# Kernel optimization log

Measured on AMD Instinct MI355X. Metric: run time of the kernel, lower is better.

The kernel has to match this reference:

```python
import jax, jax.numpy as jnp
import numpy as np

EPS = 1e-6
K_STEPS = 4
USE_GATING = True


def layer_norm(x, gamma, beta):
    mu = jnp.mean(x, axis=-1, keepdims=True)
    var = jnp.mean(jnp.square(x - mu), axis=-1, keepdims=True)
    return (x - mu) * jax.lax.rsqrt(var + EPS) * gamma + beta


def setup_inputs() -> dict:
    key = jax.random.key(0)
    B, L, D, H = 4, 4096, 2048, 8192
    ks = jax.random.split(key, 16)
    s = 0.02
    return {
        "x": jax.random.normal(ks[0], (B, L, D), dtype=jnp.float32),
        "in_gamma": jnp.ones((D,), jnp.float32),
        "in_beta": jnp.zeros((D,), jnp.float32),
        "agg_w": jax.random.normal(ks[1], (D, D), jnp.float32) * s,
        "agg_b": jnp.zeros((D,), jnp.float32),
        "pn_gamma": jnp.ones((D,), jnp.float32),
        "pn_beta": jnp.zeros((D,), jnp.float32),
        "d1_w": jax.random.normal(ks[2], (D, H), jnp.float32) * s,
        "d1_b": jnp.zeros((H,), jnp.float32),
        "d2_w": jax.random.normal(ks[3], (H, D), jnp.float32) * s,
        "d2_b": jnp.zeros((D,), jnp.float32),
        "bc_w": jax.random.normal(ks[4], (D, D), jnp.float32) * s,
        "bc_b": jnp.zeros((D,), jnp.float32),
        "gate_w": jax.random.normal(ks[5], (D, D), jnp.float32) * s,
        "gate_b": jnp.zeros((D,), jnp.float32),
        "out_gamma": jnp.ones((D,), jnp.float32),
        "out_beta": jnp.zeros((D,), jnp.float32),
    }


def reference(x, in_gamma, in_beta, agg_w, agg_b, pn_gamma, pn_beta,
              d1_w, d1_b, d2_w, d2_b, bc_w, bc_b, gate_w, gate_b,
              out_gamma, out_beta):
    # Input norm over the full sequence, then extract last-position summary.
    x_norm = layer_norm(x, in_gamma, in_beta)              # [B, L, D]
    thought = x_norm[:, -1, :] @ agg_w + agg_b             # [B, D]

    # Iterative pre-norm MLP thought refinement (fixed small k -> unrolled).
    for _ in range(K_STEPS):
        t = layer_norm(thought, pn_gamma, pn_beta)
        t = jax.nn.gelu(t @ d1_w + d1_b, approximate=False)
        thought = thought + (t @ d2_w + d2_b)

    # Broadcast refined thought back to every position.
    broadcast = (thought @ bc_w + bc_b)[:, None, :]        # [B, 1, D]

    if USE_GATING:
        gate = jax.nn.sigmoid(x @ gate_w + gate_b)         # [B, L, D]
        out = x + gate * broadcast
    else:
        out = x + broadcast
    return layer_norm(out, out_gamma, out_beta)
```

## Files before the change

kernel.cpp:

```cpp
#include <hip/hip_runtime.h>
#include <stdint.h>

typedef __attribute__((ext_vector_type(8))) short short8;
typedef __attribute__((ext_vector_type(4))) float f32x4;
typedef __attribute__((ext_vector_type(4))) unsigned short us4;

__device__ inline unsigned short f2bf(float f) {
    unsigned u = __float_as_uint(f);
    u = (u + 0x7FFFu + ((u >> 16) & 1u)) >> 16;
    return (unsigned short)u;
}

__device__ inline float bf2f(unsigned short u) {
    return __uint_as_float(((unsigned)u) << 16);
}

__device__ inline float gelu_f(float v) {
    return 0.5f * v * (1.0f + erff(v * 0.70710678118654752f));
}

__device__ inline void gload_lds16(const unsigned short* g, const unsigned short* l) {
    __builtin_amdgcn_global_load_lds(
        (const __attribute__((address_space(1))) unsigned int*)(g),
        (__attribute__((address_space(3))) unsigned int*)(l),
        16, 0, 0);
}

__global__ __launch_bounds__(256) void cvt_x_kernel(const float* __restrict__ in,
                                                    unsigned short* __restrict__ out, int n4) {
    int i = blockIdx.x * 256 + threadIdx.x;
    if (i >= n4) return;
    float4 v = reinterpret_cast<const float4*>(in)[i];
    us4 o = { f2bf(v.x), f2bf(v.y), f2bf(v.z), f2bf(v.w) };
    reinterpret_cast<us4*>(out)[i] = o;
}

__global__ __launch_bounds__(256) void transpose_w_kernel(const float* __restrict__ W,
                                                          unsigned short* __restrict__ WT,
                                                          int K, int N) {
    __shared__ float tile[32][33];
    int bn = blockIdx.x * 32;
    int bk = blockIdx.y * 32;
    int tx = threadIdx.x & 31;
    int ty = threadIdx.x >> 5;
#pragma unroll
    for (int j = 0; j < 32; j += 8)
        tile[ty + j][tx] = W[(long long)(bk + ty + j) * N + bn + tx];
    __syncthreads();
#pragma unroll
    for (int j = 0; j < 32; j += 8)
        WT[(long long)(bn + ty + j) * K + bk + tx] = f2bf(tile[tx][ty + j]);
}

__device__ inline void block_reduce2(float& s, float& q) {
#pragma unroll
    for (int o = 32; o > 0; o >>= 1) {
        s += __shfl_xor(s, o, 64);
        q += __shfl_xor(q, o, 64);
    }
    __shared__ float sh[8];
    __syncthreads();
    int w = threadIdx.x >> 6;
    if ((threadIdx.x & 63) == 0) { sh[w] = s; sh[4 + w] = q; }
    __syncthreads();
    s = (sh[0] + sh[1]) + (sh[2] + sh[3]);
    q = (sh[4] + sh[5]) + (sh[6] + sh[7]);
}

__global__ __launch_bounds__(256) void ln_rows_kernel(const float* __restrict__ in, long long in_stride,
                                                      float* __restrict__ out, long long out_stride,
                                                      const float* __restrict__ gamma,
                                                      const float* __restrict__ beta) {
    const float* p = in + (long long)blockIdx.x * in_stride;
    float* q = out + (long long)blockIdx.x * out_stride;
    int t = threadIdx.x;
    float4 a = reinterpret_cast<const float4*>(p)[t];
    float4 c = reinterpret_cast<const float4*>(p)[t + 256];
    float s  = (a.x + a.y) + (a.z + a.w) + (c.x + c.y) + (c.z + c.w);
    float ss = a.x*a.x + a.y*a.y + a.z*a.z + a.w*a.w
             + c.x*c.x + c.y*c.y + c.z*c.z + c.w*c.w;
    block_reduce2(s, ss);
    const float inv = 1.0f / 2048.0f;
    float mu = s * inv;
    float var = ss * inv - mu * mu;
    float rs = rsqrtf(var + 1e-6f);
    float4 g0 = reinterpret_cast<const float4*>(gamma)[t];
    float4 g1 = reinterpret_cast<const float4*>(gamma)[t + 256];
    float4 b0 = reinterpret_cast<const float4*>(beta)[t];
    float4 b1 = reinterpret_cast<const float4*>(beta)[t + 256];
    float4 o0, o1;
    o0.x = (a.x - mu) * rs * g0.x + b0.x;
    o0.y = (a.y - mu) * rs * g0.y + b0.y;
    o0.z = (a.z - mu) * rs * g0.z + b0.z;
    o0.w = (a.w - mu) * rs * g0.w + b0.w;
    o1.x = (c.x - mu) * rs * g1.x + b1.x;
    o1.y = (c.y - mu) * rs * g1.y + b1.y;
    o1.z = (c.z - mu) * rs * g1.z + b1.z;
    o1.w = (c.w - mu) * rs * g1.w + b1.w;
    reinterpret_cast<float4*>(q)[t] = o0;
    reinterpret_cast<float4*>(q)[t + 256] = o1;
}

template<int MODE>
__global__ __launch_bounds__(256) void gemv4f_kernel(const float* __restrict__ src, long long sstride,
                                                     const float* __restrict__ gamma,
                                                     const float* __restrict__ beta,
                                                     const float* __restrict__ W,
                                                     const float* __restrict__ bias,
                                                     float* __restrict__ out,
                                                     int K, int N, int KC) {
    __shared__ float sA[4][128];
    const int tid = threadIdx.x;
    const int k0 = blockIdx.y * KC;

    float mu[4], rsd[4];
    if (MODE == 1) {
#pragma unroll
        for (int r = 0; r < 4; ++r) {
            const float* p = src + r * sstride;
            float s = 0.f, q = 0.f;
            for (int k = tid; k < K; k += 256) { float v = p[k]; s += v; q += v * v; }
            block_reduce2(s, q);
            float m = s / K;
            mu[r] = m;
            rsd[r] = rsqrtf(q / K - m * m + 1e-6f);
        }
    }
    for (int idx = tid; idx < 4 * KC; idx += 256) {
        int r = idx / KC, k = idx - r * KC;
        float v = src[r * sstride + k0 + k];
        if (MODE == 1) v = (v - mu[r]) * rsd[r] * gamma[k0 + k] + beta[k0 + k];
        if (MODE == 2) v = gelu_f(v);
        sA[r][k] = v;
    }
    __syncthreads();

    const int n4 = blockIdx.x * 256 + tid;
    const int n = n4 * 4;
    const float4* W4 = reinterpret_cast<const float4*>(W);
    float4 a0 = {0.f, 0.f, 0.f, 0.f}, a1 = a0, a2 = a0, a3 = a0;
#pragma unroll 4
    for (int k = 0; k < KC; ++k) {
        float4 w = W4[((long long)(k0 + k) * N + n) >> 2];
        float c0 = sA[0][k], c1 = sA[1][k], c2 = sA[2][k], c3 = sA[3][k];
        a0.x = fmaf(c0, w.x, a0.x); a0.y = fmaf(c0, w.y, a0.y);
        a0.z = fmaf(c0, w.z, a0.z); a0.w = fmaf(c0, w.w, a0.w);
        a1.x = fmaf(c1, w.x, a1.x); a1.y = fmaf(c1, w.y, a1.y);
        a1.z = fmaf(c1, w.z, a1.z); a1.w = fmaf(c1, w.w, a1.w);
        a2.x = fmaf(c2, w.x, a2.x); a2.y = fmaf(c2, w.y, a2.y);
        a2.z = fmaf(c2, w.z, a2.z); a2.w = fmaf(c2, w.w, a2.w);
        a3.x = fmaf(c3, w.x, a3.x); a3.y = fmaf(c3, w.y, a3.y);
        a3.z = fmaf(c3, w.z, a3.z); a3.w = fmaf(c3, w.w, a3.w);
    }
    if (blockIdx.y == 0) {
        float4 b = reinterpret_cast<const float4*>(bias)[n4];
        a0.x += b.x; a0.y += b.y; a0.z += b.z; a0.w += b.w;
        a1.x += b.x; a1.y += b.y; a1.z += b.z; a1.w += b.w;
        a2.x += b.x; a2.y += b.y; a2.z += b.z; a2.w += b.w;
        a3.x += b.x; a3.y += b.y; a3.z += b.z; a3.w += b.w;
    }
    atomicAdd(&out[n + 0], a0.x); atomicAdd(&out[n + 1], a0.y);
    atomicAdd(&out[n + 2], a0.z); atomicAdd(&out[n + 3], a0.w);
    atomicAdd(&out[N + n + 0], a1.x); atomicAdd(&out[N + n + 1], a1.y);
    atomicAdd(&out[N + n + 2], a1.z); atomicAdd(&out[N + n + 3], a1.w);
    atomicAdd(&out[2 * N + n + 0], a2.x); atomicAdd(&out[2 * N + n + 1], a2.y);
    atomicAdd(&out[2 * N + n + 2], a2.z); atomicAdd(&out[2 * N + n + 3], a2.w);
    atomicAdd(&out[3 * N + n + 0], a3.x); atomicAdd(&out[3 * N + n + 1], a3.y);
    atomicAdd(&out[3 * N + n + 2], a3.z); atomicAdd(&out[3 * N + n + 3], a3.w);
}

#define BK 64
__global__ __launch_bounds__(512, 4) void gate_gemm_kernel(const unsigned short* __restrict__ A,
                                                           const unsigned short* __restrict__ BT,
                                                           const float* __restrict__ gate_b,
                                                           const float* __restrict__ bcast,
                                                           float* __restrict__ pre,
                                                           int M, int N, int K) {
    extern __shared__ unsigned short lds[];
    const int tid = threadIdx.x;
    const int lane = tid & 63;
    const int wave = tid >> 6;
    const int wm = wave >> 2;
    const int wn = wave & 3;
    const int bn0 = blockIdx.x * 128;
    const int bm0 = blockIdx.y * 128;
    const int NT = K / BK;

    const int ch0 = tid, ch1 = tid + 512;
    const int r0 = ch0 >> 3, c0s = (ch0 & 7) ^ (r0 & 7);
    const int r1 = ch1 >> 3, c1s = (ch1 & 7) ^ (r1 & 7);
    const int srcoff0 = r0 * K + c0s * 8;
    const int srcoff1 = r1 * K + c1s * 8;
    const int ldso0 = ch0 * 8;
    const int ldso1 = ch1 * 8;

    const unsigned short* Abase = A + (long long)bm0 * K;
    const unsigned short* Bbase = BT + (long long)bn0 * K;

#define STAGE_A(buf, t)  do { \
        const unsigned short* g = Abase + (t) * BK; \
        const unsigned short* d = &lds[(buf) * 8192]; \
        gload_lds16(g + srcoff0, d + ldso0); \
        gload_lds16(g + srcoff1, d + ldso1); } while (0)
#define STAGE_B(buf, t)  do { \
        const unsigned short* g = Bbase + (t) * BK; \
        const unsigned short* d = &lds[16384 + (buf) * 8192]; \
        gload_lds16(g + srcoff0, d + ldso0); \
        gload_lds16(g + srcoff1, d + ldso1); } while (0)

    f32x4 acc[4][2];
#pragma unroll
    for (int i = 0; i < 4; ++i)
#pragma unroll
        for (int j = 0; j < 2; ++j)
#pragma unroll
            for (int r = 0; r < 4; ++r) acc[i][j][r] = 0.f;

    const int r16 = lane & 15, kq = lane >> 4;

    STAGE_A(0, 0); STAGE_B(0, 0);
    asm volatile("s_waitcnt vmcnt(0)" ::: "memory");
    __builtin_amdgcn_s_barrier();

    for (int t = 0; t < NT; ++t) {
        const int p = t & 1;
        const int u = t + 1;
        const int a_base = p * 8192;
        const int b_base = 16384 + p * 8192;

        if (u < NT) { STAGE_A(1 - p, u); STAGE_B(1 - p, u); }
        __builtin_amdgcn_sched_barrier(0);

        short8 bf[2][2];
#pragma unroll
        for (int ni = 0; ni < 2; ++ni) {
            const int rl = wn * 32 + ni * 16 + r16;
#pragma unroll
            for (int kk = 0; kk < 2; ++kk)
                bf[ni][kk] = *reinterpret_cast<const short8*>(
                    &lds[b_base + rl * 64 + (((kk << 2) | kq) ^ (rl & 7)) * 8]);
        }
        short8 af[4][2];
#pragma unroll
        for (int mi = 0; mi < 4; ++mi) {
            const int rl = wm * 64 + mi * 16 + r16;
#pragma unroll
            for (int kk = 0; kk < 2; ++kk)
                af[mi][kk] = *reinterpret_cast<const short8*>(
                    &lds[a_base + rl * 64 + (((kk << 2) | kq) ^ (rl & 7)) * 8]);
        }
        __builtin_amdgcn_s_setprio(1);
#pragma unroll
        for (int mi = 0; mi < 4; ++mi)
#pragma unroll
            for (int ni = 0; ni < 2; ++ni)
#pragma unroll
                for (int kk = 0; kk < 2; ++kk)
                    acc[mi][ni] = __builtin_amdgcn_mfma_f32_16x16x32_bf16(
                        af[mi][kk], bf[ni][kk], acc[mi][ni], 0, 0, 0);
        __builtin_amdgcn_s_setprio(0);
        asm volatile("s_waitcnt vmcnt(0)" ::: "memory");
        __builtin_amdgcn_s_barrier();
    }

    const int bnum = bm0 >> 12;
    const float* bc_row = bcast + (long long)bnum * N;
#pragma unroll
    for (int mi = 0; mi < 4; ++mi) {
        const int row = bm0 + wm * 64 + mi * 16 + kq * 4;
#pragma unroll
        for (int ni = 0; ni < 2; ++ni) {
            const int col = bn0 + wn * 32 + ni * 16 + r16;
            const float gb = gate_b[col];
            const float bc = bc_row[col];
#pragma unroll
            for (int r = 0; r < 4; ++r) {
                const long long off = (long long)(row + r) * N + col;
                const float v = acc[mi][ni][r] + gb;
                const float g = 1.0f / (1.0f + __expf(-v));
                pre[off] = bf2f(A[off]) + g * bc;
            }
        }
    }
}
#undef STAGE_A
#undef STAGE_B

extern "C" void kernel_launch(void* const* d_in, const int* in_sizes, int n_in,
                              void* d_out, int out_size, void* d_ws, size_t ws_size,
                              hipStream_t stream) {
    const float* x         = (const float*)d_in[0];
    const float* in_gamma  = (const float*)d_in[1];
    const float* in_beta   = (const float*)d_in[2];
    const float* agg_w     = (const float*)d_in[3];
    const float* agg_b     = (const float*)d_in[4];
    const float* pn_gamma  = (const float*)d_in[5];
    const float* pn_beta   = (const float*)d_in[6];
    const float* d1_w      = (const float*)d_in[7];
    const float* d1_b      = (const float*)d_in[8];
    const float* d2_w      = (const float*)d_in[9];
    const float* d2_b      = (const float*)d_in[10];
    const float* bc_w      = (const float*)d_in[11];
    const float* bc_b      = (const float*)d_in[12];
    const float* gate_w    = (const float*)d_in[13];
    const float* gate_b    = (const float*)d_in[14];
    const float* out_gamma = (const float*)d_in[15];
    const float* out_beta  = (const float*)d_in[16];

    const int B = 4, L = 4096, D = 2048, H = 8192;
    const int M = B * L;
    float* out = (float*)d_out;

    char* ws = (char*)d_ws;
    unsigned short* xb  = (unsigned short*)ws;
    unsigned short* gwT = (unsigned short*)(ws + 67108864);
    float* tbuf  = (float*)(ws + 75497472);
    float* bcast = tbuf + 4 * D;
    float* hbuf0 = bcast + 4 * D;

    static bool attr_done = false;
    if (!attr_done) {
        hipFuncSetAttribute((const void*)gate_gemm_kernel,
                            hipFuncAttributeMaxDynamicSharedMemorySize, 65536);
        attr_done = true;
    }

    hipMemsetAsync(tbuf, 0, (4 * D + 4 * D + 4 * 4 * H) * sizeof(float), stream);

    gemv4f_kernel<1><<<dim3(D / 1024, 64), dim3(256), 0, stream>>>(
        x + (long long)(L - 1) * D, (long long)L * D, in_gamma, in_beta,
        agg_w, agg_b, tbuf, D, D, 32);

    for (int s = 0; s < 4; ++s) {
        float* hbuf = hbuf0 + s * 4 * H;
        gemv4f_kernel<1><<<dim3(H / 1024, 32), dim3(256), 0, stream>>>(
            tbuf, (long long)D, pn_gamma, pn_beta, d1_w, d1_b, hbuf, D, H, 64);
        gemv4f_kernel<2><<<dim3(D / 1024, 128), dim3(256), 0, stream>>>(
            hbuf, (long long)H, nullptr, nullptr, d2_w, d2_b, tbuf, H, D, 64);
    }
    gemv4f_kernel<0><<<dim3(D / 1024, 64), dim3(256), 0, stream>>>(
        tbuf, (long long)D, nullptr, nullptr, bc_w, bc_b, bcast, D, D, 32);

    cvt_x_kernel<<<dim3((M * D / 4) / 256), dim3(256), 0, stream>>>(x, xb, M * D / 4);
    transpose_w_kernel<<<dim3(D / 32, D / 32), dim3(256), 0, stream>>>(gate_w, gwT, D, D);

    gate_gemm_kernel<<<dim3(D / 128, M / 128), dim3(512), 65536, stream>>>(
        xb, gwT, gate_b, bcast, out, M, D, D);

    ln_rows_kernel<<<dim3(M), dim3(256), 0, stream>>>(
        out, (long long)D, out, (long long)D, out_gamma, out_beta);
}
```

Measured before the change: 539.0 us.

## Replace d1 atomics with partial-sum buffers and remap gate GEMM blocks per XCD

The d1 GEMV now writes per-K-chunk partial sums with plain stores instead of atomicAdd. The following d2 GEMV reduces those 32 partials, adds the bias and applies GELU while loading. This also shrinks the memset, since the hidden buffers no longer need zeroing. Separately, the gate GEMM uses a 1D grid with a block-index swizzle so consecutive blocks on the same XCD share A rows, aiming for better L2 reuse; the cost is more reads in the d2 prologue.

```diff
diff --git a/kernel.cpp b/kernel.cpp
--- a/kernel.cpp
+++ b/kernel.cpp
@@ -101,10 +101,11 @@
     reinterpret_cast<float4*>(q)[t + 256] = o1;
 }
 
-template<int MODE>
+template<int MODE, int PARTIAL>
 __global__ __launch_bounds__(256) void gemv4f_kernel(const float* __restrict__ src, long long sstride,
                                                      const float* __restrict__ gamma,
                                                      const float* __restrict__ beta,
+                                                     const float* __restrict__ srcbias, int nY,
                                                      const float* __restrict__ W,
                                                      const float* __restrict__ bias,
                                                      float* __restrict__ out,
@@ -113,8 +114,8 @@
     const int tid = threadIdx.x;
     const int k0 = blockIdx.y * KC;
 
-    float mu[4], rsd[4];
     if (MODE == 1) {
+        float mu[4], rsd[4];
 #pragma unroll
         for (int r = 0; r < 4; ++r) {
             const float* p = src + r * sstride;
@@ -125,13 +126,25 @@
             mu[r] = m;
             rsd[r] = rsqrtf(q / K - m * m + 1e-6f);
         }
-    }
-    for (int idx = tid; idx < 4 * KC; idx += 256) {
-        int r = idx / KC, k = idx - r * KC;
-        float v = src[r * sstride + k0 + k];
-        if (MODE == 1) v = (v - mu[r]) * rsd[r] * gamma[k0 + k] + beta[k0 + k];
-        if (MODE == 2) v = gelu_f(v);
-        sA[r][k] = v;
+        for (int idx = tid; idx < 4 * KC; idx += 256) {
+            int r = idx / KC, k = idx - r * KC;
+            float v = src[r * sstride + k0 + k];
+            sA[r][k] = (v - mu[r]) * rsd[r] * gamma[k0 + k] + beta[k0 + k];
+        }
+    } else if (MODE == 3) {
+        for (int idx = tid; idx < 4 * KC; idx += 256) {
+            int r = idx / KC, k = idx - r * KC;
+            float acc = srcbias[k0 + k];
+#pragma unroll 8
+            for (int y = 0; y < nY; ++y)
+                acc += src[((long long)(y * 4 + r)) * sstride + k0 + k];
+            sA[r][k] = gelu_f(acc);
+        }
+    } else {
+        for (int idx = tid; idx < 4 * KC; idx += 256) {
+            int r = idx / KC, k = idx - r * KC;
+            sA[r][k] = src[r * sstride + k0 + k];
+        }
     }
     __syncthreads();
 
@@ -152,6 +165,17 @@
         a3.x = fmaf(c3, w.x, a3.x); a3.y = fmaf(c3, w.y, a3.y);
         a3.z = fmaf(c3, w.z, a3.z); a3.w = fmaf(c3, w.w, a3.w);
     }
+
+    if (PARTIAL) {
+        float4* P4 = reinterpret_cast<float4*>(out);
+        const long long pb = (long long)blockIdx.y * 4 * N;
+        P4[(pb + 0 * N + n) >> 2] = a0;
+        P4[(pb + 1 * N + n) >> 2] = a1;
+        P4[(pb + 2 * N + n) >> 2] = a2;
+        P4[(pb + 3 * N + n) >> 2] = a3;
+        return;
+    }
+
     if (blockIdx.y == 0) {
         float4 b = reinterpret_cast<const float4*>(bias)[n4];
         a0.x += b.x; a0.y += b.y; a0.z += b.z; a0.w += b.w;
@@ -182,8 +206,13 @@
     const int wave = tid >> 6;
     const int wm = wave >> 2;
     const int wn = wave & 3;
-    const int bn0 = blockIdx.x * 128;
-    const int bm0 = blockIdx.y * 128;
+
+    const int bid = blockIdx.x;
+    const int xcd = bid & 7, seq = bid >> 3;
+    const int mp = (seq >> 4) * 8 + xcd;
+    const int np = seq & 15;
+    const int bm0 = mp * 128;
+    const int bn0 = np * 128;
     const int NT = K / BK;
 
     const int ch0 = tid, ch1 = tid + 512;
@@ -316,7 +345,7 @@
     unsigned short* gwT = (unsigned short*)(ws + 67108864);
     float* tbuf  = (float*)(ws + 75497472);
     float* bcast = tbuf + 4 * D;
-    float* hbuf0 = bcast + 4 * D;
+    float* P1    = bcast + 4 * D;
 
     static bool attr_done = false;
     if (!attr_done) {
@@ -325,26 +354,25 @@
         attr_done = true;
     }
 
-    hipMemsetAsync(tbuf, 0, (4 * D + 4 * D + 4 * 4 * H) * sizeof(float), stream);
-
-    gemv4f_kernel<1><<<dim3(D / 1024, 64), dim3(256), 0, stream>>>(
+    hipMemsetAsync(tbuf, 0, 8 * D * sizeof(float), stream);
+
+    gemv4f_kernel<1, 0><<<dim3(D / 1024, 64), dim3(256), 0, stream>>>(
         x + (long long)(L - 1) * D, (long long)L * D, in_gamma, in_beta,
-        agg_w, agg_b, tbuf, D, D, 32);
+        nullptr, 0, agg_w, agg_b, tbuf, D, D, 32);
 
     for (int s = 0; s < 4; ++s) {
-        float* hbuf = hbuf0 + s * 4 * H;
-        gemv4f_kernel<1><<<dim3(H / 1024, 32), dim3(256), 0, stream>>>(
-            tbuf, (long long)D, pn_gamma, pn_beta, d1_w, d1_b, hbuf, D, H, 64);
-        gemv4f_kernel<2><<<dim3(D / 1024, 128), dim3(256), 0, stream>>>(
-            hbuf, (long long)H, nullptr, nullptr, d2_w, d2_b, tbuf, H, D, 64);
-    }
-    gemv4f_kernel<0><<<dim3(D / 1024, 64), dim3(256), 0, stream>>>(
-        tbuf, (long long)D, nullptr, nullptr, bc_w, bc_b, bcast, D, D, 32);
+        gemv4f_kernel<1, 1><<<dim3(H / 1024, 32), dim3(256), 0, stream>>>(
+            tbuf, (long long)D, pn_gamma, pn_beta, nullptr, 0, d1_w, nullptr, P1, D, H, 64);
+        gemv4f_kernel<3, 0><<<dim3(D / 1024, 128), dim3(256), 0, stream>>>(
+            P1, (long long)H, nullptr, nullptr, d1_b, 32, d2_w, d2_b, tbuf, H, D, 64);
+    }
+    gemv4f_kernel<0, 0><<<dim3(D / 1024, 64), dim3(256), 0, stream>>>(
+        tbuf, (long long)D, nullptr, nullptr, nullptr, 0, bc_w, bc_b, bcast, D, D, 32);
 
     cvt_x_kernel<<<dim3((M * D / 4) / 256), dim3(256), 0, stream>>>(x, xb, M * D / 4);
     transpose_w_kernel<<<dim3(D / 32, D / 32), dim3(256), 0, stream>>>(gate_w, gwT, D, D);
 
-    gate_gemm_kernel<<<dim3(D / 128, M / 128), dim3(512), 65536, stream>>>(
+    gate_gemm_kernel<<<dim3((M / 128) * (D / 128)), dim3(512), 65536, stream>>>(
         xb, gwT, gate_b, bcast, out, M, D, D);
 
     ln_rows_kernel<<<dim3(M), dim3(256), 0, stream>>>(
```

New measurement: 495.9 us. 1.09x faster.
